# Optimization experiments

Hardware: AMD Instinct MI355X
Metric: run time of the kernel (lower is better)

## Reference

```python
import jax, jax.numpy as jnp
import numpy as np

N, M, D = 8192, 8192, 256

def setup_inputs() -> dict:
    key = jax.random.key(0)
    k1, k2, k3, k4 = jax.random.split(key, 4)
    x1 = jax.random.normal(k1, (N, D), dtype=jnp.float32)
    x2 = jax.random.normal(k2, (M, D), dtype=jnp.float32)
    alpha_raw = jax.random.normal(k3, (D,), dtype=jnp.float32)      # nn.Parameter(torch.randn(input_dim))
    variance_raw = jnp.ones((1,), dtype=jnp.float32)                # nn.Parameter(torch.ones(1))
    return {"x1": x1, "x2": x2, "alpha_raw": alpha_raw, "variance_raw": variance_raw}

def reference(x1, x2, alpha_raw, variance_raw):
    # alpha = softmax(alpha_raw^2), variance = variance_raw^2
    alpha = jax.nn.softmax(alpha_raw ** 2)                          # (D,)
    variance = variance_raw ** 2                                    # (1,)
    # GEMM rewrite of sum_d alpha_d (x1_i - x2_j)^2:
    #   ||x1*sqrt(a)||^2 - 2 (x1*sqrt(a))(x2*sqrt(a))^T + ||x2*sqrt(a)||^2
    sa = jnp.sqrt(alpha)
    a = x1 * sa                                                     # (N, D)
    b = x2 * sa                                                     # (M, D)
    sq = (jnp.sum(a * a, axis=-1)[:, None]
          - 2.0 * (a @ b.T)
          + jnp.sum(b * b, axis=-1)[None, :])                       # (N, M)
    sq = jnp.maximum(sq, 0.0)  # numerical guard; exact value is non-negative
    kernel = variance * jnp.exp(-0.5 * sq)                          # (N, M)
    if kernel.shape[0] == 1:
        kernel = jnp.squeeze(kernel)
    return kernel
```

## Files before the change

kernel.cpp:

```cpp
#include <hip/hip_runtime.h>
#include <stdint.h>

#define NROWS 8192
#define MCOLS 8192
#define KDIM  256

typedef __bf16 bf16x8 __attribute__((ext_vector_type(8)));
typedef float  floatx4 __attribute__((ext_vector_type(4)));

__device__ __forceinline__ unsigned short f32_to_bf16_rne(float f) {
    unsigned int u = __float_as_uint(f);
    u += 0x7FFFu + ((u >> 16) & 1u);
    return (unsigned short)(u >> 16);
}
__device__ __forceinline__ float bf16_to_f32(unsigned short h) {
    return __uint_as_float(((unsigned int)h) << 16);
}

__device__ __forceinline__ void async16(const void* g, void* l) {
    __builtin_amdgcn_global_load_lds(
        (const __attribute__((address_space(1))) unsigned int*)g,
        (__attribute__((address_space(3))) unsigned int*)l,
        16, 0, 0);
}

__global__ void prep_alpha(const float* __restrict__ araw, float* __restrict__ sa) {
    int d = threadIdx.x;
    float z = araw[d];
    z = z * z;
    float m = z;
#pragma unroll
    for (int off = 32; off; off >>= 1) m = fmaxf(m, __shfl_xor(m, off));
    __shared__ float wred[4];
    if ((d & 63) == 0) wred[d >> 6] = m;
    __syncthreads();
    float mx = fmaxf(fmaxf(wred[0], wred[1]), fmaxf(wred[2], wred[3]));
    float e = __expf(z - mx);
    float s = e;
#pragma unroll
    for (int off = 32; off; off >>= 1) s += __shfl_xor(s, off);
    __syncthreads();
    if ((d & 63) == 0) wred[d >> 6] = s;
    __syncthreads();
    float sum = wred[0] + wred[1] + wred[2] + wred[3];
    sa[d] = sqrtf(e / sum);
}

__global__ void prep_rows(const float* __restrict__ x1, const float* __restrict__ x2,
                          const float* __restrict__ sa,
                          unsigned short* __restrict__ Amat, unsigned short* __restrict__ Bmat,
                          float* __restrict__ ra, float* __restrict__ rb) {
    int blk = blockIdx.x;
    const float* x; unsigned short* mat; float* nrm; int row;
    if (blk < NROWS) { x = x1; mat = Amat; nrm = ra; row = blk; }
    else             { x = x2; mat = Bmat; nrm = rb; row = blk - NROWS; }
    int d = threadIdx.x;
    float v = x[(size_t)row * KDIM + d] * sa[d];
    unsigned short h = f32_to_bf16_rne(v);
    mat[(size_t)row * KDIM + d] = h;
    float fv = bf16_to_f32(h);
    float p = fv * fv;
#pragma unroll
    for (int off = 32; off; off >>= 1) p += __shfl_xor(p, off);
    __shared__ float wred[4];
    if ((d & 63) == 0) wred[d >> 6] = p;
    __syncthreads();
    if (d == 0) nrm[row] = wred[0] + wred[1] + wred[2] + wred[3];
}

__global__ __launch_bounds__(256) void rbf_gemm(
    const unsigned short* __restrict__ A, const unsigned short* __restrict__ B,
    const float* __restrict__ ra, const float* __restrict__ rb,
    const float* __restrict__ vraw, float* __restrict__ out)
{
    __shared__ unsigned short As[2][128 * 64];
    __shared__ unsigned short Bs[2][128 * 64];

    const int tid  = threadIdx.x;
    const int lane = tid & 63;
    const int wave = tid >> 6;

    const int g   = blockIdx.y * gridDim.x + blockIdx.x;
    const int xcd = g & 7;
    const int i   = g >> 3;
    const int bm  = (xcd >> 2) * 32 + (i >> 4);
    const int bn  = (xcd & 3) * 16 + (i & 15);

    const int wm = (wave & 1) * 64;
    const int wn = (wave >> 1) * 64;
    const int quad = lane >> 4;
    const int l15  = lane & 15;

    floatx4 acc[4][4];
#pragma unroll
    for (int tj = 0; tj < 4; tj++)
#pragma unroll
        for (int ti = 0; ti < 4; ti++) acc[tj][ti] = (floatx4)0.0f;

    auto stage = [&](int buf, int k0) {
#pragma unroll
        for (int it = 0; it < 4; ++it) {
            int c   = it * 256 + tid;
            int row = c >> 3;
            int kc  = c & 7;
            int gkc = kc ^ (row & 7);
            const unsigned short* gA = A + (size_t)(bm * 128 + row) * KDIM + k0 + gkc * 8;
            const unsigned short* gB = B + (size_t)(bn * 128 + row) * KDIM + k0 + gkc * 8;
            async16(gA, &As[buf][c * 8]);
            async16(gB, &Bs[buf][c * 8]);
        }
    };

    stage(0, 0);
    __syncthreads();

#pragma unroll
    for (int t = 0; t < 4; ++t) {
        if (t < 3) stage((t + 1) & 1, (t + 1) * 64);
        const unsigned short* Ab = As[t & 1];
        const unsigned short* Bb = Bs[t & 1];
#pragma unroll
        for (int ks = 0; ks < 2; ++ks) {
            bf16x8 af[4], bfr[4];
            int kc = ks * 4 + quad;
#pragma unroll
            for (int tt = 0; tt < 4; ++tt) {
                int m   = wm + tt * 16 + l15;
                int sA  = m * 8 + (kc ^ (m & 7));
                af[tt]  = *(const bf16x8*)&Ab[sA * 8];
                int n   = wn + tt * 16 + l15;
                int sB  = n * 8 + (kc ^ (n & 7));
                bfr[tt] = *(const bf16x8*)&Bb[sB * 8];
            }
#pragma unroll
            for (int tj = 0; tj < 4; ++tj)
#pragma unroll
                for (int ti = 0; ti < 4; ++ti)
                    acc[tj][ti] = __builtin_amdgcn_mfma_f32_16x16x32_bf16(
                        bfr[tj], af[ti], acc[tj][ti], 0, 0, 0);
        }
        if (t < 3) __syncthreads();
    }

    float variance = vraw[0] * vraw[0];
#pragma unroll
    for (int ti = 0; ti < 4; ++ti) {
        int row = bm * 128 + wm + ti * 16 + l15;
        float rav = ra[row];
        float* orow = out + (size_t)row * MCOLS;
#pragma unroll
        for (int tj = 0; tj < 4; ++tj) {
            int nbase = bn * 128 + wn + tj * 16 + quad * 4;
            floatx4 rbv = *(const floatx4*)&rb[nbase];
            floatx4 val;
#pragma unroll
            for (int r = 0; r < 4; ++r) {
                float s = rav + rbv[r] - 2.0f * acc[tj][ti][r];
                s = fmaxf(s, 0.0f);
                val[r] = variance * __expf(-0.5f * s);
            }
            *(floatx4*)&orow[nbase] = val;
        }
    }
}

extern "C" void kernel_launch(void* const* d_in, const int* in_sizes, int n_in,
                              void* d_out, int out_size, void* d_ws, size_t ws_size,
                              hipStream_t stream) {
    const float* x1   = (const float*)d_in[0];
    const float* x2   = (const float*)d_in[1];
    const float* araw = (const float*)d_in[2];
    const float* vraw = (const float*)d_in[3];
    float* out = (float*)d_out;

    char* ws = (char*)d_ws;
    float* sa = (float*)ws;
    float* ra = (float*)(ws + 1024);
    float* rb = (float*)(ws + 1024 + 32768);
    unsigned short* Amat = (unsigned short*)(ws + 66560);
    unsigned short* Bmat = (unsigned short*)(ws + 66560 + (size_t)NROWS * KDIM * 2);

    prep_alpha<<<1, 256, 0, stream>>>(araw, sa);
    prep_rows<<<NROWS + MCOLS, 256, 0, stream>>>(x1, x2, sa, Amat, Bmat, ra, rb);

    dim3 grid(MCOLS / 128, NROWS / 128);
    rbf_gemm<<<grid, 256, 0, stream>>>(Amat, Bmat, ra, rb, vraw, out);
}
```

Before: 313.0 us.

## Single-buffer GEMM LDS tiles and process one row per wave in prep

The GEMM drops its double-buffered LDS staging for a single buffer. This halves shared memory per block so more blocks can be resident per CU, but loads and MFMA work are no longer overlapped within a block. The row-prep kernel now handles one row per wavefront with float4 loads and 4-wide bf16 stores. That removes the cross-wave LDS reduction and its __syncthreads, and launches a quarter as many blocks.

```diff
diff --git a/kernel.cpp b/kernel.cpp
--- a/kernel.cpp
+++ b/kernel.cpp
@@ -7,6 +7,7 @@
 
 typedef __bf16 bf16x8 __attribute__((ext_vector_type(8)));
 typedef float  floatx4 __attribute__((ext_vector_type(4)));
+typedef unsigned short ushort4v __attribute__((ext_vector_type(4)));
 
 __device__ __forceinline__ unsigned short f32_to_bf16_rne(float f) {
     unsigned int u = __float_as_uint(f);
@@ -50,22 +51,29 @@
                           const float* __restrict__ sa,
                           unsigned short* __restrict__ Amat, unsigned short* __restrict__ Bmat,
                           float* __restrict__ ra, float* __restrict__ rb) {
-    int blk = blockIdx.x;
+    int wave = threadIdx.x >> 6;
+    int lane = threadIdx.x & 63;
+    int grow = blockIdx.x * 4 + wave;
     const float* x; unsigned short* mat; float* nrm; int row;
-    if (blk < NROWS) { x = x1; mat = Amat; nrm = ra; row = blk; }
-    else             { x = x2; mat = Bmat; nrm = rb; row = blk - NROWS; }
-    int d = threadIdx.x;
-    float v = x[(size_t)row * KDIM + d] * sa[d];
-    unsigned short h = f32_to_bf16_rne(v);
-    mat[(size_t)row * KDIM + d] = h;
-    float fv = bf16_to_f32(h);
-    float p = fv * fv;
+    if (grow < NROWS) { x = x1; mat = Amat; nrm = ra; row = grow; }
+    else              { x = x2; mat = Bmat; nrm = rb; row = grow - NROWS; }
+
+    floatx4 v  = *(const floatx4*)&x[(size_t)row * KDIM + lane * 4];
+    floatx4 sv = *(const floatx4*)&sa[lane * 4];
+    ushort4v h;
+    float p = 0.0f;
+#pragma unroll
+    for (int j = 0; j < 4; ++j) {
+        float f = v[j] * sv[j];
+        unsigned short hh = f32_to_bf16_rne(f);
+        h[j] = hh;
+        float fv = bf16_to_f32(hh);
+        p += fv * fv;
+    }
+    *(ushort4v*)&mat[(size_t)row * KDIM + lane * 4] = h;
 #pragma unroll
     for (int off = 32; off; off >>= 1) p += __shfl_xor(p, off);
-    __shared__ float wred[4];
-    if ((d & 63) == 0) wred[d >> 6] = p;
-    __syncthreads();
-    if (d == 0) nrm[row] = wred[0] + wred[1] + wred[2] + wred[3];
+    if (lane == 0) nrm[row] = p;
 }
 
 __global__ __launch_bounds__(256) void rbf_gemm(
@@ -73,8 +81,8 @@
     const float* __restrict__ ra, const float* __restrict__ rb,
     const float* __restrict__ vraw, float* __restrict__ out)
 {
-    __shared__ unsigned short As[2][128 * 64];
-    __shared__ unsigned short Bs[2][128 * 64];
+    __shared__ unsigned short As[128 * 64];
+    __shared__ unsigned short Bs[128 * 64];
 
     const int tid  = threadIdx.x;
     const int lane = tid & 63;
@@ -97,7 +105,8 @@
 #pragma unroll
         for (int ti = 0; ti < 4; ti++) acc[tj][ti] = (floatx4)0.0f;
 
-    auto stage = [&](int buf, int k0) {
+    for (int t = 0; t < 4; ++t) {
+        int k0 = t * 64;
 #pragma unroll
         for (int it = 0; it < 4; ++it) {
             int c   = it * 256 + tid;
@@ -106,19 +115,11 @@
             int gkc = kc ^ (row & 7);
             const unsigned short* gA = A + (size_t)(bm * 128 + row) * KDIM + k0 + gkc * 8;
             const unsigned short* gB = B + (size_t)(bn * 128 + row) * KDIM + k0 + gkc * 8;
-            async16(gA, &As[buf][c * 8]);
-            async16(gB, &Bs[buf][c * 8]);
+            async16(gA, &As[c * 8]);
+            async16(gB, &Bs[c * 8]);
         }
-    };
+        __syncthreads();
 
-    stage(0, 0);
-    __syncthreads();
-
-#pragma unroll
-    for (int t = 0; t < 4; ++t) {
-        if (t < 3) stage((t + 1) & 1, (t + 1) * 64);
-        const unsigned short* Ab = As[t & 1];
-        const unsigned short* Bb = Bs[t & 1];
 #pragma unroll
         for (int ks = 0; ks < 2; ++ks) {
             bf16x8 af[4], bfr[4];
@@ -127,10 +128,10 @@
             for (int tt = 0; tt < 4; ++tt) {
                 int m   = wm + tt * 16 + l15;
                 int sA  = m * 8 + (kc ^ (m & 7));
-                af[tt]  = *(const bf16x8*)&Ab[sA * 8];
+                af[tt]  = *(const bf16x8*)&As[sA * 8];
                 int n   = wn + tt * 16 + l15;
                 int sB  = n * 8 + (kc ^ (n & 7));
-                bfr[tt] = *(const bf16x8*)&Bb[sB * 8];
+                bfr[tt] = *(const bf16x8*)&Bs[sB * 8];
             }
 #pragma unroll
             for (int tj = 0; tj < 4; ++tj)
@@ -181,7 +182,7 @@
     unsigned short* Bmat = (unsigned short*)(ws + 66560 + (size_t)NROWS * KDIM * 2);
 
     prep_alpha<<<1, 256, 0, stream>>>(araw, sa);
-    prep_rows<<<NROWS + MCOLS, 256, 0, stream>>>(x1, x2, sa, Amat, Bmat, ra, rb);
+    prep_rows<<<(NROWS + MCOLS) / 4, 256, 0, stream>>>(x1, x2, sa, Amat, Bmat, ra, rb);
 
     dim3 grid(MCOLS / 128, NROWS / 128);
     rbf_gemm<<<grid, 256, 0, stream>>>(Amat, Bmat, ra, rb, vraw, out);
```

New measurement: 304.6 us. 2.7% less time.
